# Kernel tuning notes

Measured on AMD Instinct MI355X. Metric: run time of the kernel, lower is better.

## Reference

```python
import jax, jax.numpy as jnp
import numpy as np

N_FEAT = 512
N_HEAD = 8
D_K = N_FEAT // N_HEAD


def setup_inputs() -> dict:
    key = jax.random.key(0)
    ks = jax.random.split(key, 10)
    B, S = 2, 4096
    scale = 1.0 / np.sqrt(N_FEAT)
    inp = {
        "x": jax.random.normal(ks[0], (B, S, N_FEAT), dtype=jnp.float32),
        "mask": jnp.zeros((B, 1, 1, S), dtype=jnp.float32),
        "wq": jax.random.normal(ks[1], (N_FEAT, N_FEAT), dtype=jnp.float32) * scale,
        "bq": jnp.zeros((N_FEAT,), dtype=jnp.float32),
        "wk": jax.random.normal(ks[2], (N_FEAT, N_FEAT), dtype=jnp.float32) * scale,
        "bk": jnp.zeros((N_FEAT,), dtype=jnp.float32),
        "wv": jax.random.normal(ks[3], (N_FEAT, N_FEAT), dtype=jnp.float32) * scale,
        "bv": jnp.zeros((N_FEAT,), dtype=jnp.float32),
        "wo": jax.random.normal(ks[4], (N_FEAT, N_FEAT), dtype=jnp.float32) * scale,
        "bo": jnp.zeros((N_FEAT,), dtype=jnp.float32),
    }
    return inp


def reference(x, mask, wq, bq, wk, bk, wv, bv, wo, bo):
    B, S, _ = x.shape
    # QKV projections (weights stored [in, out] = W^T of torch Linear)
    def proj(w, b):
        y = x @ w + b                      # [B, S, n_feat]
        y = y.reshape(B, S, N_HEAD, D_K)
        return y.transpose(0, 2, 1, 3)     # [B, H, S, d_k]
    q = proj(wq, bq)
    k = proj(wk, bk)
    v = proj(wv, bv)
    scores = jnp.einsum("bhsd,bhtd->bhst", q, k) / jnp.sqrt(jnp.float32(D_K))
    scores = scores + mask                 # additive mask, broadcast [B,1,1,S]
    attn = jax.nn.softmax(scores, axis=-1) # [B, H, S, S]
    ctx = jnp.einsum("bhst,bhtd->bhsd", attn, v)
    ctx = ctx.transpose(0, 2, 1, 3).reshape(B, S, N_FEAT)
    return ctx @ wo + bo
```

## Files before the change

### kernel.cpp

```cpp
#include <hip/hip_runtime.h>
#include <hip/hip_bf16.h>
#include <math.h>

#define SLEN 4096
#define NF   512
#define LOG2E 1.44269504f

typedef short s8v  __attribute__((ext_vector_type(8)));
typedef short s4v  __attribute__((ext_vector_type(4)));
typedef float f4v  __attribute__((ext_vector_type(4)));
typedef float f16v __attribute__((ext_vector_type(16)));

static __device__ __forceinline__ short f2bf(float f) {
  union { float f; unsigned int u; } v; v.f = f;
  unsigned int u = v.u;
  unsigned int r = (u + 0x7FFFu + ((u >> 16) & 1u)) >> 16;
  return (short)r;
}

__global__ __launch_bounds__(256) void prep_x(const float* __restrict__ x,
                                              short* __restrict__ xb) {
  size_t i = ((size_t)blockIdx.x * 256 + threadIdx.x) * 8;
  float4 a = *(const float4*)(x + i);
  float4 b = *(const float4*)(x + i + 4);
  s8v o;
  o[0] = f2bf(a.x); o[1] = f2bf(a.y); o[2] = f2bf(a.z); o[3] = f2bf(a.w);
  o[4] = f2bf(b.x); o[5] = f2bf(b.y); o[6] = f2bf(b.z); o[7] = f2bf(b.w);
  *(s8v*)(xb + i) = o;
}

__global__ __launch_bounds__(256) void prep_w(
    const float* __restrict__ wq, const float* __restrict__ wk,
    const float* __restrict__ wv, const float* __restrict__ wo,
    short* __restrict__ wt) {
  const int bz = blockIdx.y;
  const float* W = (bz == 0) ? wq : (bz == 1) ? wk : (bz == 2) ? wv : wo;
  const float scale = (bz == 0) ? 0.125f * LOG2E : 1.0f;
  const int tk = blockIdx.x & 7, tn = blockIdx.x >> 3;
  __shared__ short T[64][68];
  const int tid = threadIdx.x;
#pragma unroll
  for (int p = 0; p < 4; p++) {
    int c = tid + 256 * p;
    int kk = c >> 4, c4 = c & 15;
    float4 v = *(const float4*)(W + (size_t)(tk * 64 + kk) * NF + tn * 64 + c4 * 4);
    T[kk][c4 * 4 + 0] = f2bf(v.x * scale);
    T[kk][c4 * 4 + 1] = f2bf(v.y * scale);
    T[kk][c4 * 4 + 2] = f2bf(v.z * scale);
    T[kk][c4 * 4 + 3] = f2bf(v.w * scale);
  }
  __syncthreads();
#pragma unroll
  for (int p = 0; p < 2; p++) {
    int c = tid + 256 * p;
    int nrow = c >> 3, ks = c & 7;
    s8v g;
#pragma unroll
    for (int j = 0; j < 8; j++) g[j] = T[ks * 8 + j][nrow];
    *(s8v*)(wt + (size_t)bz * NF * NF + (size_t)(tn * 64 + nrow) * NF + tk * 64 + ks * 8) = g;
  }
}

__global__ __launch_bounds__(256) void prep_misc(
    const float* __restrict__ bq, const float* __restrict__ mask,
    float* __restrict__ bqs, float* __restrict__ maskl) {
  const int tid = threadIdx.x;
#pragma unroll
  for (int j = 0; j < 2; j++) {
    int i = tid + 256 * j;
    bqs[i] = bq[i] * (0.125f * LOG2E);
  }
#pragma unroll
  for (int j = 0; j < 8; j++) {
    int i4 = (j * 256 + tid) * 4;
    float4 m = *(const float4*)(mask + i4);
    m.x *= LOG2E; m.y *= LOG2E; m.z *= LOG2E; m.w *= LOG2E;
    *(float4*)(maskl + i4) = m;
  }
}

__global__ __launch_bounds__(256) void qkv_proj(
    const short* __restrict__ xb, const short* __restrict__ wt,
    const float* __restrict__ bqs, const float* __restrict__ bk,
    const float* __restrict__ bv,
    short* __restrict__ qo, short* __restrict__ ko, short* __restrict__ vo)
{
  const int z = blockIdx.z;
  const short* WT   = wt + (size_t)z * NF * NF;
  const float* bias = (z == 0) ? bqs : (z == 1) ? bk : bv;
  const int m0 = blockIdx.x * 128;
  const int n0 = blockIdx.y * 128;

  __shared__ short Al[128][32];
  __shared__ short Bl[128][32];

  const int tid = threadIdx.x;
  const int wave = tid >> 6, lane = tid & 63;
  const int lg = lane >> 4, lr = lane & 15;
  const int wm = wave >> 1, wn = wave & 1;

  f4v acc[4][4];
#pragma unroll
  for (int i = 0; i < 4; i++)
#pragma unroll
    for (int j = 0; j < 4; j++) acc[i][j] = (f4v){0.f, 0.f, 0.f, 0.f};

  for (int k0 = 0; k0 < NF; k0 += 32) {
    __syncthreads();
#pragma unroll
    for (int i = 0; i < 2; i++) {
      int c = tid + 256 * i;
      int row = c >> 2, sl = c & 3;
      *(s8v*)&Al[row][sl * 8] = *(const s8v*)(xb + (size_t)(m0 + row) * NF + k0 + sl * 8);
      *(s8v*)&Bl[row][sl * 8] = *(const s8v*)(WT + (size_t)(n0 + row) * NF + k0 + sl * 8);
    }
    __syncthreads();

    s8v af[4], bf[4];
#pragma unroll
    for (int f = 0; f < 4; f++) af[f] = *(const s8v*)&Al[wm * 64 + f * 16 + lr][lg * 8];
#pragma unroll
    for (int f = 0; f < 4; f++) bf[f] = *(const s8v*)&Bl[wn * 64 + f * 16 + lr][lg * 8];
#pragma unroll
    for (int i = 0; i < 4; i++)
#pragma unroll
      for (int j = 0; j < 4; j++)
        acc[i][j] = __builtin_amdgcn_mfma_f32_16x16x32_bf16(af[i], bf[j], acc[i][j], 0, 0, 0);
  }

#pragma unroll
  for (int i = 0; i < 4; i++) {
    int mbase = m0 + wm * 64 + i * 16 + lg * 4;
#pragma unroll
    for (int j = 0; j < 4; j++) {
      int n = n0 + wn * 64 + j * 16 + lr;
      float bval = bias[n];
      int h = n >> 6, d = n & 63;
      if (z == 2) {
        int b = mbase >> 12, s = mbase & 4095;
        s4v pk;
#pragma unroll
        for (int r = 0; r < 4; r++) pk[r] = f2bf(acc[i][j][r] + bval);
        *(s4v*)(vo + ((size_t)((b * 8 + h) * 64 + d)) * SLEN + s) = pk;
      } else {
        short* dst = (z == 0) ? qo : ko;
#pragma unroll
        for (int r = 0; r < 4; r++) {
          int m = mbase + r;
          int b = m >> 12, s = m & 4095;
          dst[((size_t)((b * 8 + h)) * SLEN + s) * 64 + d] = f2bf(acc[i][j][r] + bval);
        }
      }
    }
  }
}

template<int SPLIT>
__global__ __launch_bounds__(256) void attn(
    const short* __restrict__ q, const short* __restrict__ k,
    const short* __restrict__ vt, const float* __restrict__ maskl,
    short* __restrict__ ctx, float* __restrict__ poa, float* __restrict__ plc)
{
  const int KVLEN = SLEN / SPLIT;
  const int NT = KVLEN / 64;
  __shared__ short Kl[2][64][64];
  __shared__ short Vl[2][64][64];

  const int tid = threadIdx.x;
  const int wave = tid >> 6, lane = tid & 63;
  const int h = lane >> 5, ln = lane & 31;
  const int bh = blockIdx.y, qb = blockIdx.x;
  const int sp = (SPLIT > 1) ? blockIdx.z : 0;
  const int bb = bh >> 3, hh = bh & 7;
  const int q0 = qb * 128 + wave * 32;

  const short* qp = q + ((size_t)bh * SLEN + q0 + ln) * 64 + h * 8;
  s8v qf[4];
#pragma unroll
  for (int d = 0; d < 4; d++) qf[d] = *(const s8v*)(qp + d * 16);

  s8v ones;
#pragma unroll
  for (int j = 0; j < 8; j++) ones[j] = (short)0x3F80;

  f16v oa[2], lacc;
#pragma unroll
  for (int i = 0; i < 16; i++) { oa[0][i] = 0.f; oa[1][i] = 0.f; lacc[i] = 0.f; }

  const short* kg = k + (size_t)bh * SLEN * 64 + (size_t)sp * KVLEN * 64;
  const short* vg = vt + (size_t)bh * 64 * SLEN + (size_t)sp * KVLEN;
  const float* mp = maskl + (size_t)bb * SLEN + (size_t)sp * KVLEN;

  const int srow = tid >> 3, ss = tid & 7;
  const int sws = (ss ^ (srow & 7)) * 8;

  s8v kr0 = *(const s8v*)(kg + (size_t)srow * 64 + ss * 8);
  s8v kr1 = *(const s8v*)(kg + (size_t)(srow + 32) * 64 + ss * 8);
  s8v vr0 = *(const s8v*)(vg + (size_t)srow * SLEN + ss * 8);
  s8v vr1 = *(const s8v*)(vg + (size_t)(srow + 32) * SLEN + ss * 8);
  *(s8v*)&Kl[0][srow][sws] = kr0;  *(s8v*)&Kl[0][srow + 32][sws] = kr1;
  *(s8v*)&Vl[0][srow][sws] = vr0;  *(s8v*)&Vl[0][srow + 32][sws] = vr1;

  for (int it = 0; it < NT; ++it) {
    const int cur = it & 1;
    const int t0 = it * 64;
    __syncthreads();

    if (it + 1 < NT) {
      kr0 = *(const s8v*)(kg + (size_t)(t0 + 64 + srow) * 64 + ss * 8);
      kr1 = *(const s8v*)(kg + (size_t)(t0 + 96 + srow) * 64 + ss * 8);
      vr0 = *(const s8v*)(vg + (size_t)srow * SLEN + t0 + 64 + ss * 8);
      vr1 = *(const s8v*)(vg + (size_t)(srow + 32) * SLEN + t0 + 64 + ss * 8);
    }

    f16v sa[2];
#pragma unroll
    for (int tt = 0; tt < 2; tt++) {
#pragma unroll
      for (int q4 = 0; q4 < 4; q4++) {
        float4 mv = *(const float4*)(mp + t0 + tt * 32 + q4 * 8 + h * 4);
        sa[tt][q4 * 4 + 0] = mv.x;
        sa[tt][q4 * 4 + 1] = mv.y;
        sa[tt][q4 * 4 + 2] = mv.z;
        sa[tt][q4 * 4 + 3] = mv.w;
      }
    }
    __builtin_amdgcn_s_setprio(1);
#pragma unroll
    for (int tt = 0; tt < 2; tt++) {
#pragma unroll
      for (int ds_ = 0; ds_ < 4; ds_++) {
        s8v kf = *(const s8v*)&Kl[cur][tt * 32 + ln][(((ds_ * 2 + h) ^ (ln & 7))) * 8];
        sa[tt] = __builtin_amdgcn_mfma_f32_32x32x16_bf16(kf, qf[ds_], sa[tt], 0, 0, 0);
      }
    }
    __builtin_amdgcn_s_setprio(0);

    unsigned int pku[2][4][2];
#pragma unroll
    for (int tt = 0; tt < 2; tt++)
#pragma unroll
      for (int q4 = 0; q4 < 4; q4++) {
        float p0, p1, p2, p3;
        asm("v_exp_f32 %0, %1" : "=v"(p0) : "v"(sa[tt][q4 * 4 + 0]));
        asm("v_exp_f32 %0, %1" : "=v"(p1) : "v"(sa[tt][q4 * 4 + 1]));
        asm("v_exp_f32 %0, %1" : "=v"(p2) : "v"(sa[tt][q4 * 4 + 2]));
        asm("v_exp_f32 %0, %1" : "=v"(p3) : "v"(sa[tt][q4 * 4 + 3]));
        unsigned int u0, u1;
        asm("v_cvt_pk_bf16_f32 %0, %1, %2" : "=v"(u0) : "v"(p0), "v"(p1));
        asm("v_cvt_pk_bf16_f32 %0, %1, %2" : "=v"(u1) : "v"(p2), "v"(p3));
        pku[tt][q4][0] = u0;
        pku[tt][q4][1] = u1;
      }

    __builtin_amdgcn_s_setprio(1);
#pragma unroll
    for (int ks = 0; ks < 4; ks++) {
      const int tt = ks >> 1, k1 = ks & 1;
      unsigned int s0 = h ? pku[tt][2 * k1][0] : pku[tt][2 * k1 + 1][0];
      unsigned int s1 = h ? pku[tt][2 * k1][1] : pku[tt][2 * k1 + 1][1];
      unsigned int r0 = (unsigned int)__shfl_xor((int)s0, 32);
      unsigned int r1 = (unsigned int)__shfl_xor((int)s1, 32);
      union { unsigned int u[4]; s8v v; } af;
      af.u[0] = h ? r0 : pku[tt][2 * k1][0];
      af.u[1] = h ? r1 : pku[tt][2 * k1][1];
      af.u[2] = h ? pku[tt][2 * k1 + 1][0] : r0;
      af.u[3] = h ? pku[tt][2 * k1 + 1][1] : r1;
      lacc = __builtin_amdgcn_mfma_f32_32x32x16_bf16(af.v, ones, lacc, 0, 0, 0);
#pragma unroll
      for (int dt = 0; dt < 2; dt++) {
        s8v vf = *(const s8v*)&Vl[cur][dt * 32 + ln][(((ks * 2 + h) ^ (ln & 7))) * 8];
        oa[dt] = __builtin_amdgcn_mfma_f32_32x32x16_bf16(af.v, vf, oa[dt], 0, 0, 0);
      }
    }
    __builtin_amdgcn_s_setprio(0);

    if (it + 1 < NT) {
      *(s8v*)&Kl[cur ^ 1][srow][sws] = kr0;  *(s8v*)&Kl[cur ^ 1][srow + 32][sws] = kr1;
      *(s8v*)&Vl[cur ^ 1][srow][sws] = vr0;  *(s8v*)&Vl[cur ^ 1][srow + 32][sws] = vr1;
    }
  }

  if constexpr (SPLIT == 1) {
#pragma unroll
    for (int q4 = 0; q4 < 4; q4++)
#pragma unroll
      for (int i = 0; i < 4; i++) {
        float inv = 1.0f / lacc[q4 * 4 + i];
        int qrow = q0 + i + q4 * 8 + 4 * h;
        size_t base = ((size_t)bb * SLEN + qrow) * NF + hh * 64;
        ctx[base + ln]      = f2bf(oa[0][q4 * 4 + i] * inv);
        ctx[base + 32 + ln] = f2bf(oa[1][q4 * 4 + i] * inv);
      }
  } else {
#pragma unroll
    for (int dt = 0; dt < 2; dt++) {
      size_t dbase = ((size_t)(sp * 16 + bh) * 64 + dt * 32 + ln) * SLEN;
#pragma unroll
      for (int q4 = 0; q4 < 4; q4++) {
        float4 v = {oa[dt][q4 * 4 + 0], oa[dt][q4 * 4 + 1],
                    oa[dt][q4 * 4 + 2], oa[dt][q4 * 4 + 3]};
        *(float4*)(poa + dbase + q0 + q4 * 8 + 4 * h) = v;
      }
    }
    if (ln == 0) {
      size_t lbase = (size_t)(sp * 16 + bh) * SLEN;
#pragma unroll
      for (int q4 = 0; q4 < 4; q4++) {
        float4 v = {lacc[q4 * 4 + 0], lacc[q4 * 4 + 1],
                    lacc[q4 * 4 + 2], lacc[q4 * 4 + 3]};
        *(float4*)(plc + lbase + q0 + q4 * 8 + 4 * h) = v;
      }
    }
  }
}

__global__ __launch_bounds__(256) void combine(
    const float* __restrict__ poa, const float* __restrict__ plc,
    short* __restrict__ ctx)
{
  const int bh = blockIdx.x, rb = blockIdx.y;
  const int bb = bh >> 3, hh = bh & 7;
  const int r0 = rb * 32;
  __shared__ short Cl[32][72];
  __shared__ float Ls[32];
  const int tid = threadIdx.x;
  if (tid < 32)
    Ls[tid] = plc[(size_t)bh * SLEN + r0 + tid] +
              plc[(size_t)(16 + bh) * SLEN + r0 + tid];
  __syncthreads();
  const int d = tid >> 2, rq = tid & 3;
#pragma unroll
  for (int l = 0; l < 2; l++) {
    int row4 = rq * 8 + l * 4;
    size_t a0 = ((size_t)bh * 64 + d) * SLEN + r0 + row4;
    size_t a1 = ((size_t)(16 + bh) * 64 + d) * SLEN + r0 + row4;
    float4 p0 = *(const float4*)(poa + a0);
    float4 p1 = *(const float4*)(poa + a1);
    Cl[row4 + 0][d] = f2bf((p0.x + p1.x) / Ls[row4 + 0]);
    Cl[row4 + 1][d] = f2bf((p0.y + p1.y) / Ls[row4 + 1]);
    Cl[row4 + 2][d] = f2bf((p0.z + p1.z) / Ls[row4 + 2]);
    Cl[row4 + 3][d] = f2bf((p0.w + p1.w) / Ls[row4 + 3]);
  }
  __syncthreads();
  int row = tid >> 3, ds8 = tid & 7;
  *(s8v*)(ctx + ((size_t)bb * SLEN + r0 + row) * NF + hh * 64 + ds8 * 8) =
      *(const s8v*)&Cl[row][ds8 * 8];
}

__global__ __launch_bounds__(256) void out_proj(
    const short* __restrict__ ctx, const short* __restrict__ wt,
    const float* __restrict__ bo, float* __restrict__ out)
{
  const short* WT = wt + (size_t)3 * NF * NF;
  const int m0 = blockIdx.x * 128;
  const int n0 = blockIdx.y * 128;
  __shared__ short Al[128][32];
  __shared__ short Bl[128][32];
  const int tid = threadIdx.x;
  const int wave = tid >> 6, lane = tid & 63;
  const int lg = lane >> 4, lr = lane & 15;
  const int wm = wave >> 1, wn = wave & 1;

  f4v acc[4][4];
#pragma unroll
  for (int i = 0; i < 4; i++)
#pragma unroll
    for (int j = 0; j < 4; j++) acc[i][j] = (f4v){0.f, 0.f, 0.f, 0.f};

  for (int k0 = 0; k0 < NF; k0 += 32) {
    __syncthreads();
#pragma unroll
    for (int i = 0; i < 2; i++) {
      int c = tid + 256 * i;
      int row = c >> 2, sl = c & 3;
      *(s8v*)&Al[row][sl * 8] = *(const s8v*)(ctx + (size_t)(m0 + row) * NF + k0 + sl * 8);
      *(s8v*)&Bl[row][sl * 8] = *(const s8v*)(WT + (size_t)(n0 + row) * NF + k0 + sl * 8);
    }
    __syncthreads();

    s8v af[4], bf[4];
#pragma unroll
    for (int f = 0; f < 4; f++) af[f] = *(const s8v*)&Al[wm * 64 + f * 16 + lr][lg * 8];
#pragma unroll
    for (int f = 0; f < 4; f++) bf[f] = *(const s8v*)&Bl[wn * 64 + f * 16 + lr][lg * 8];
#pragma unroll
    for (int i = 0; i < 4; i++)
#pragma unroll
      for (int j = 0; j < 4; j++)
        acc[i][j] = __builtin_amdgcn_mfma_f32_16x16x32_bf16(af[i], bf[j], acc[i][j], 0, 0, 0);
  }

#pragma unroll
  for (int i = 0; i < 4; i++) {
    int mbase = m0 + wm * 64 + i * 16 + lg * 4;
#pragma unroll
    for (int j = 0; j < 4; j++) {
      int n = n0 + wn * 64 + j * 16 + lr;
      float bval = bo[n];
#pragma unroll
      for (int r = 0; r < 4; r++)
        out[(size_t)(mbase + r) * NF + n] = acc[i][j][r] + bval;
    }
  }
}

extern "C" void kernel_launch(void* const* d_in, const int* in_sizes, int n_in,
                              void* d_out, int out_size, void* d_ws, size_t ws_size,
                              hipStream_t stream) {
  const float* x    = (const float*)d_in[0];
  const float* mask = (const float*)d_in[1];
  const float* wq   = (const float*)d_in[2];
  const float* bq   = (const float*)d_in[3];
  const float* wk   = (const float*)d_in[4];
  const float* bk   = (const float*)d_in[5];
  const float* wv   = (const float*)d_in[6];
  const float* bv   = (const float*)d_in[7];
  const float* wo   = (const float*)d_in[8];
  const float* bo   = (const float*)d_in[9];
  float* out = (float*)d_out;

  char* ws = (char*)d_ws;
  const size_t MB = 1024ull * 1024ull;
  short* xb    = (short*)(ws);
  short* q_ws  = (short*)(ws + 8 * MB);
  short* k_ws  = (short*)(ws + 16 * MB);
  short* v_ws  = (short*)(ws + 24 * MB);
  short* c_ws  = (short*)(ws + 32 * MB);
  short* wt    = (short*)(ws + 40 * MB);
  float* bqs   = (float*)(ws + 42 * MB);
  float* maskl = (float*)(ws + 43 * MB);
  float* poa   = (float*)(ws + 44 * MB);
  float* plc   = (float*)(ws + 76 * MB);
  const size_t NEED_SPLIT = 77 * MB;

  prep_x<<<2048, 256, 0, stream>>>(x, xb);
  prep_w<<<dim3(64, 4), 256, 0, stream>>>(wq, wk, wv, wo, wt);
  prep_misc<<<1, 256, 0, stream>>>(bq, mask, bqs, maskl);
  qkv_proj<<<dim3(64, 4, 3), 256, 0, stream>>>(xb, wt, bqs, bk, bv, q_ws, k_ws, v_ws);
  if (ws_size >= NEED_SPLIT) {
    attn<2><<<dim3(32, 16, 2), 256, 0, stream>>>(q_ws, k_ws, v_ws, maskl, c_ws, poa, plc);
    combine<<<dim3(16, 128), 256, 0, stream>>>(poa, plc, c_ws);
  } else {
    attn<1><<<dim3(32, 16, 1), 256, 0, stream>>>(q_ws, k_ws, v_ws, maskl, c_ws, poa, plc);
  }
  out_proj<<<dim3(64, 4), 256, 0, stream>>>(c_ws, wt, bo, out);
}
```

Baseline: 174.6 us.

## Stage mask in LDS, remap attention grid for XCD locality, interleave score/exp

The attention kernel now preloads its slice of the additive mask into shared memory once per block and reads it from LDS each tile instead of from global memory. The grid becomes 1-D and block indices are remapped so that blocks with the same (batch, head, split) land on the same XCD (index modulo 8), aiming to improve L2 reuse of K/V. The QK^T MFMA and the exp/convert work are now interleaved per 32-column tile, which shortens the live range of the score accumulators. The cost is extra LDS (8KB for SPLIT=2, 16KB for SPLIT=1), which may reduce occupancy.

New measurement: 176.4 us. No clear change (+1.1%).

```diff
diff --git a/kernel.cpp b/kernel.cpp
--- a/kernel.cpp
+++ b/kernel.cpp
@@ -165,12 +165,18 @@
   const int NT = KVLEN / 64;
   __shared__ short Kl[2][64][64];
   __shared__ short Vl[2][64][64];
+  __shared__ float Ml[SLEN / SPLIT];
 
   const int tid = threadIdx.x;
   const int wave = tid >> 6, lane = tid & 63;
   const int h = lane >> 5, ln = lane & 31;
-  const int bh = blockIdx.y, qb = blockIdx.x;
-  const int sp = (SPLIT > 1) ? blockIdx.z : 0;
+
+  const int x = blockIdx.x;
+  const int c8 = x & 7, idx = x >> 3;
+  const int bhsp = c8 + 8 * (idx >> 5);
+  const int qb = idx & 31;
+  const int bh = bhsp & 15;
+  const int sp = bhsp >> 4;
   const int bb = bh >> 3, hh = bh & 7;
   const int q0 = qb * 128 + wave * 32;
 
@@ -190,6 +196,10 @@
   const short* kg = k + (size_t)bh * SLEN * 64 + (size_t)sp * KVLEN * 64;
   const short* vg = vt + (size_t)bh * 64 * SLEN + (size_t)sp * KVLEN;
   const float* mp = maskl + (size_t)bb * SLEN + (size_t)sp * KVLEN;
+
+#pragma unroll
+  for (int i = tid; i < KVLEN / 4; i += 256)
+    *(float4*)&Ml[i * 4] = *(const float4*)(mp + i * 4);
 
   const int srow = tid >> 3, ss = tid & 7;
   const int sws = (ss ^ (srow & 7)) * 8;
@@ -213,45 +223,39 @@
       vr1 = *(const s8v*)(vg + (size_t)(srow + 32) * SLEN + t0 + 64 + ss * 8);
     }
 
-    f16v sa[2];
+    unsigned int pku[2][4][2];
 #pragma unroll
     for (int tt = 0; tt < 2; tt++) {
+      f16v sa;
 #pragma unroll
       for (int q4 = 0; q4 < 4; q4++) {
-        float4 mv = *(const float4*)(mp + t0 + tt * 32 + q4 * 8 + h * 4);
-        sa[tt][q4 * 4 + 0] = mv.x;
-        sa[tt][q4 * 4 + 1] = mv.y;
-        sa[tt][q4 * 4 + 2] = mv.z;
-        sa[tt][q4 * 4 + 3] = mv.w;
-      }
-    }
-    __builtin_amdgcn_s_setprio(1);
-#pragma unroll
-    for (int tt = 0; tt < 2; tt++) {
+        float4 mv = *(const float4*)&Ml[t0 + tt * 32 + q4 * 8 + h * 4];
+        sa[q4 * 4 + 0] = mv.x;
+        sa[q4 * 4 + 1] = mv.y;
+        sa[q4 * 4 + 2] = mv.z;
+        sa[q4 * 4 + 3] = mv.w;
+      }
+      __builtin_amdgcn_s_setprio(1);
 #pragma unroll
       for (int ds_ = 0; ds_ < 4; ds_++) {
         s8v kf = *(const s8v*)&Kl[cur][tt * 32 + ln][(((ds_ * 2 + h) ^ (ln & 7))) * 8];
-        sa[tt] = __builtin_amdgcn_mfma_f32_32x32x16_bf16(kf, qf[ds_], sa[tt], 0, 0, 0);
-      }
-    }
-    __builtin_amdgcn_s_setprio(0);
-
-    unsigned int pku[2][4][2];
-#pragma unroll
-    for (int tt = 0; tt < 2; tt++)
+        sa = __builtin_amdgcn_mfma_f32_32x32x16_bf16(kf, qf[ds_], sa, 0, 0, 0);
+      }
+      __builtin_amdgcn_s_setprio(0);
 #pragma unroll
       for (int q4 = 0; q4 < 4; q4++) {
         float p0, p1, p2, p3;
-        asm("v_exp_f32 %0, %1" : "=v"(p0) : "v"(sa[tt][q4 * 4 + 0]));
-        asm("v_exp_f32 %0, %1" : "=v"(p1) : "v"(sa[tt][q4 * 4 + 1]));
-        asm("v_exp_f32 %0, %1" : "=v"(p2) : "v"(sa[tt][q4 * 4 + 2]));
-        asm("v_exp_f32 %0, %1" : "=v"(p3) : "v"(sa[tt][q4 * 4 + 3]));
+        asm("v_exp_f32 %0, %1" : "=v"(p0) : "v"(sa[q4 * 4 + 0]));
+        asm("v_exp_f32 %0, %1" : "=v"(p1) : "v"(sa[q4 * 4 + 1]));
+        asm("v_exp_f32 %0, %1" : "=v"(p2) : "v"(sa[q4 * 4 + 2]));
+        asm("v_exp_f32 %0, %1" : "=v"(p3) : "v"(sa[q4 * 4 + 3]));
         unsigned int u0, u1;
         asm("v_cvt_pk_bf16_f32 %0, %1, %2" : "=v"(u0) : "v"(p0), "v"(p1));
         asm("v_cvt_pk_bf16_f32 %0, %1, %2" : "=v"(u1) : "v"(p2), "v"(p3));
         pku[tt][q4][0] = u0;
         pku[tt][q4][1] = u1;
       }
+    }
 
     __builtin_amdgcn_s_setprio(1);
 #pragma unroll
@@ -439,10 +443,10 @@
   prep_misc<<<1, 256, 0, stream>>>(bq, mask, bqs, maskl);
   qkv_proj<<<dim3(64, 4, 3), 256, 0, stream>>>(xb, wt, bqs, bk, bv, q_ws, k_ws, v_ws);
   if (ws_size >= NEED_SPLIT) {
-    attn<2><<<dim3(32, 16, 2), 256, 0, stream>>>(q_ws, k_ws, v_ws, maskl, c_ws, poa, plc);
+    attn<2><<<1024, 256, 0, stream>>>(q_ws, k_ws, v_ws, maskl, c_ws, poa, plc);
     combine<<<dim3(16, 128), 256, 0, stream>>>(poa, plc, c_ws);
   } else {
-    attn<1><<<dim3(32, 16, 1), 256, 0, stream>>>(q_ws, k_ws, v_ws, maskl, c_ws, poa, plc);
+    attn<1><<<512, 256, 0, stream>>>(q_ws, k_ws, v_ws, maskl, c_ws, poa, plc);
   }
   out_proj<<<dim3(64, 4), 256, 0, stream>>>(c_ws, wt, bo, out);
 }
```
